# Kernel optimization log

Measured on AMD Instinct MI355X. Metric: run time of the kernel, lower is better.

Reference implementation:

```python
import jax, jax.numpy as jnp
import numpy as np

N_DENSE = 13
N_SPARSE = 26
FIELD_FEAT = 10000
FIELD_NUM = N_DENSE + N_SPARSE  # 39
FEATURE_NUM = N_DENSE + N_SPARSE * FIELD_FEAT  # 260013
K = 16
BATCH = 4096


def setup_inputs() -> dict:
    key = jax.random.key(0)
    k1, k2, k3, k4 = jax.random.split(key, 4)
    dense = jax.random.uniform(k1, (BATCH, N_DENSE), dtype=jnp.float32)
    sparse = jax.random.randint(k2, (BATCH, N_SPARSE), 0, FIELD_FEAT).astype(jnp.float32)
    x = jnp.concatenate([dense, sparse], axis=1)  # [B, field_num]
    # xavier-ish scale for embeddings
    W = jax.random.normal(k3, (FIELD_NUM, FEATURE_NUM, K), dtype=jnp.float32) * 0.01
    fc_w = jax.random.normal(k4, (FEATURE_NUM, 1), dtype=jnp.float32) * 0.01
    bias = jnp.zeros((1,), dtype=jnp.float32)
    field_features = np.array([1] * N_DENSE + [FIELD_FEAT] * N_SPARSE)
    offsets = jnp.asarray(np.concatenate([[0], np.cumsum(field_features)[:-1]]), dtype=jnp.int32)
    return {"x": x, "W": W, "fc_w": fc_w, "bias": bias, "offsets": offsets, "n_dense": N_DENSE}


def reference(x, W, fc_w, bias, offsets, n_dense):
    B, F = x.shape
    # build global feature indices: dense columns -> index 0 (+offset), sparse keep value
    idx = jnp.floor(x).astype(jnp.int32)
    idx = idx.at[:, :n_dense].set(0)
    x_f = idx + offsets[None, :]  # [B, F]
    # field-aware gather: E[i, b, j] = W[i][x_f[b, j]]  -> [F, B, F, K]
    E = jnp.take(W, x_f, axis=1)
    # pairwise dots: dot[b, i, j] = <E[i, b, j], E[j, b, i]>
    dot = jnp.einsum('ibjk,jbik->bij', E, E)  # [B, F, F]
    # multiplier: dense value for dense fields, 1 for sparse fields
    x_m = jnp.concatenate([x[:, :n_dense], jnp.ones((B, F - n_dense), dtype=x.dtype)], axis=1)
    w_pair = x_m[:, :, None] * x_m[:, None, :]  # [B, F, F]
    # original loops: i in [0, F-2], j in [0, F-1] (full j range, faithfully kept)
    row_mask = (jnp.arange(F) < F - 1).astype(x.dtype)[None, :, None]  # [1, F, 1]
    cross = jnp.sum(dot * w_pair * row_mask, axis=(1, 2), keepdims=False)[:, None]  # [B, 1]
    linear = jnp.sum(fc_w[x_f], axis=1) + bias  # [B, 1]
    return jax.nn.sigmoid(linear + cross)
```

## Files before the change

kernel.cpp:

```cpp
#include <hip/hip_runtime.h>
#include <math.h>

#define NF 39
#define ND 13
#define KDIM 16
#define FEAT 260013
#define NPAIRS (NF * (NF + 1) / 2)
#define PASSES ((NPAIRS + 31) / 32)

__global__ __launch_bounds__(256) void ffm_kernel(
    const float* __restrict__ x,
    const float* __restrict__ W,
    const float* __restrict__ fc_w,
    const float* __restrict__ bias,
    const int*   __restrict__ offsets,
    float* __restrict__ out,
    int B)
{
    __shared__ int            sf[NF];
    __shared__ float          sxm[NF];
    __shared__ unsigned short spij[NPAIRS];
    __shared__ float          sred[4];

    const int b   = blockIdx.x;
    const int tid = threadIdx.x;

    if (tid < NF) {
        float xv = x[(size_t)b * NF + tid];
        int idx  = (tid < ND) ? 0 : (int)floorf(xv);
        sf[tid]  = idx + offsets[tid];
        sxm[tid] = (tid < ND) ? xv : 1.0f;
    }
    for (int p = tid; p < NPAIRS; p += 256) {
        int i = 0, base = 0;
        while (p >= base + (NF - i)) { base += NF - i; ++i; }
        int j = i + (p - base);
        spij[p] = (unsigned short)(i | (j << 8));
    }
    __syncthreads();

    const int slot = tid >> 3;
    const int quad = (tid >> 2) & 1;
    const int qi   = tid & 3;

    float acc = 0.0f;
    if (tid < NF) acc += fc_w[sf[tid]];

    #pragma unroll 5
    for (int pass = 0; pass < PASSES; ++pass) {
        int p  = pass * 32 + slot;
        int pc = (p < NPAIRS) ? p : (NPAIRS - 1);
        int ij = spij[pc];
        int i  = ij & 0xff;
        int j  = ij >> 8;

        float w;
        if (i == j)            w = (i < NF - 1) ? sxm[i] * sxm[i] : 0.0f;
        else if (j < NF - 1)   w = 2.0f * sxm[i] * sxm[j];
        else                   w = sxm[i] * sxm[j];
        if (p >= NPAIRS) w = 0.0f;

        int row  = quad ? j : i;
        int feat = quad ? sf[i] : sf[j];
        const float4* vp = (const float4*)(W + ((size_t)row * FEAT + feat) * KDIM);
        float4 v = vp[qi];

        float4 u;
        u.x = __shfl_xor(v.x, 4, 64);
        u.y = __shfl_xor(v.y, 4, 64);
        u.z = __shfl_xor(v.z, 4, 64);
        u.w = __shfl_xor(v.w, 4, 64);

        float d = v.x * u.x + v.y * u.y + v.z * u.z + v.w * u.w;
        acc += 0.5f * w * d;
    }

    #pragma unroll
    for (int off = 32; off > 0; off >>= 1)
        acc += __shfl_down(acc, off, 64);
    if ((tid & 63) == 0) sred[tid >> 6] = acc;
    __syncthreads();

    if (tid == 0) {
        float z = sred[0] + sred[1] + sred[2] + sred[3] + bias[0];
        out[b] = 1.0f / (1.0f + expf(-z));
    }
}

extern "C" void kernel_launch(void* const* d_in, const int* in_sizes, int n_in,
                              void* d_out, int out_size, void* d_ws, size_t ws_size,
                              hipStream_t stream) {
    const float* x       = (const float*)d_in[0];
    const float* W       = (const float*)d_in[1];
    const float* fc_w    = (const float*)d_in[2];
    const float* bias    = (const float*)d_in[3];
    const int*   offsets = (const int*)d_in[4];

    float* out = (float*)d_out;
    const int B = in_sizes[0] / NF;

    ffm_kernel<<<B, 256, 0, stream>>>(x, W, fc_w, bias, offsets, out, B);
}
```

Baseline: 781.3 us.

## Transpose embedding table to feature-major layout before the FFM gather

Adds a kernel that rewrites W from field-major [39][FEAT][16] into feature-major [FEAT][39][16] in the workspace. The main kernel can then load each sparse feature's full 39-field embedding row as one contiguous 2.5KB chunk into shared memory, instead of issuing many scattered 64-byte gathers. Pair weights are precomputed into shared memory and each pair is handled by 4 lanes with float4 loads. The cost is a full read and write of the roughly 650MB table on every call, and the new path only runs when the workspace is large enough. Otherwise it falls back to the old kernel.

```diff
diff --git a/kernel.cpp b/kernel.cpp
--- a/kernel.cpp
+++ b/kernel.cpp
@@ -3,19 +3,140 @@
 
 #define NF 39
 #define ND 13
+#define NS 26
 #define KDIM 16
 #define FEAT 260013
 #define NPAIRS (NF * (NF + 1) / 2)
-#define PASSES ((NPAIRS + 31) / 32)
-
-__global__ __launch_bounds__(256) void ffm_kernel(
+
+#define ROWF4 4
+#define CHUNKF4 (NF * ROWF4)
+#define CHUNKF4_PAD 157
+#define PAIR_SLOTS 832
+#define CPASSES 13
+#define TFEAT 26
+#define TROWF4 (TFEAT * ROWF4)
+#define TROWF4_PAD 105
+
+__global__ __launch_bounds__(256) void ffm_transpose(
+    const float4* __restrict__ W4,
+    float4* __restrict__ WT4)
+{
+    __shared__ float4 sT[NF * TROWF4_PAD];
+    const int fbase = blockIdx.x * TFEAT;
+    const int tid   = threadIdx.x;
+
+    #pragma unroll 8
+    for (int r = tid; r < NF * TROWF4; r += 256) {
+        int row = r / TROWF4;
+        int w   = r - row * TROWF4;
+        if (fbase + (w >> 2) < FEAT)
+            sT[row * TROWF4_PAD + w] = W4[((size_t)row * FEAT + fbase) * 4 + w];
+    }
+    __syncthreads();
+
+    #pragma unroll 8
+    for (int o = tid; o < TFEAT * CHUNKF4; o += 256) {
+        int fl  = o / CHUNKF4;
+        int rem = o - fl * CHUNKF4;
+        int i   = rem >> 2;
+        int k4  = rem & 3;
+        int f   = fbase + fl;
+        if (f < FEAT)
+            WT4[(size_t)f * CHUNKF4 + rem] = sT[i * TROWF4_PAD + (fl << 2) + k4];
+    }
+}
+
+__global__ __launch_bounds__(256) void ffm_main(
     const float* __restrict__ x,
-    const float* __restrict__ W,
+    const float4* __restrict__ WT4,
     const float* __restrict__ fc_w,
     const float* __restrict__ bias,
     const int*   __restrict__ offsets,
     float* __restrict__ out,
     int B)
+{
+    __shared__ float4         sC[NS * CHUNKF4_PAD];
+    __shared__ int            sgb[NF];
+    __shared__ int            sfeat[NF];
+    __shared__ float          sxm[NF];
+    __shared__ unsigned short spij[PAIR_SLOTS];
+    __shared__ float          sw[PAIR_SLOTS];
+    __shared__ float          sred[4];
+
+    const int b   = blockIdx.x;
+    const int tid = threadIdx.x;
+
+    if (tid < NF) {
+        float xv   = x[(size_t)b * NF + tid];
+        int idx    = (tid < ND) ? 0 : (int)floorf(xv);
+        int f      = idx + offsets[tid];
+        sfeat[tid] = f;
+        sgb[tid]   = f * CHUNKF4;
+        sxm[tid]   = (tid < ND) ? xv : 1.0f;
+    }
+    __syncthreads();
+
+    float acc = 0.0f;
+    if (tid < NF) acc += fc_w[sfeat[tid]];
+
+    for (int p = tid; p < PAIR_SLOTS; p += 256) {
+        int i = 0, j = 0; float w = 0.0f;
+        if (p < NPAIRS) {
+            int base = 0, ii = 0;
+            while (p >= base + (NF - ii)) { base += NF - ii; ++ii; }
+            i = ii; j = ii + (p - base);
+            if (i == j)          w = (i < NF - 1) ? sxm[i] * sxm[i] : 0.0f;
+            else if (j < NF - 1) w = 2.0f * sxm[i] * sxm[j];
+            else                 w = sxm[i] * sxm[j];
+        }
+        spij[p] = (unsigned short)(i | (j << 8));
+        sw[p]   = w;
+    }
+
+    #pragma unroll 8
+    for (int t = tid; t < NS * CHUNKF4; t += 256) {
+        int c = t / CHUNKF4;
+        int w = t - c * CHUNKF4;
+        sC[c * CHUNKF4_PAD + w] = WT4[(size_t)sgb[ND + c] + w];
+    }
+    __syncthreads();
+
+    const int slot = tid >> 2;
+    const int q    = tid & 3;
+
+    #pragma unroll 4
+    for (int pass = 0; pass < CPASSES; ++pass) {
+        int   p   = pass * 64 + slot;
+        int   ij  = spij[p];
+        int   i   = ij & 0xff;
+        int   j   = ij >> 8;
+        float wgt = sw[p];
+
+        float4 a = (j >= ND) ? sC[(j - ND) * CHUNKF4_PAD + (i << 2) + q]
+                             : WT4[(size_t)sgb[j] + (i << 2) + q];
+        float4 v = (i >= ND) ? sC[(i - ND) * CHUNKF4_PAD + (j << 2) + q]
+                             : WT4[(size_t)sgb[i] + (j << 2) + q];
+
+        acc += wgt * (a.x * v.x + a.y * v.y + a.z * v.z + a.w * v.w);
+    }
+
+    #pragma unroll
+    for (int off = 32; off > 0; off >>= 1)
+        acc += __shfl_down(acc, off, 64);
+    if ((tid & 63) == 0) sred[tid >> 6] = acc;
+    __syncthreads();
+
+    if (tid == 0) {
+        float z = sred[0] + sred[1] + sred[2] + sred[3] + bias[0];
+        out[b] = 1.0f / (1.0f + expf(-z));
+    }
+}
+
+#define PASSES ((NPAIRS + 31) / 32)
+__global__ __launch_bounds__(256) void ffm_kernel(
+    const float* __restrict__ x, const float* __restrict__ W,
+    const float* __restrict__ fc_w, const float* __restrict__ bias,
+    const int* __restrict__ offsets, float* __restrict__ out, int B)
 {
     __shared__ int            sf[NF];
     __shared__ float          sxm[NF];
@@ -55,9 +176,9 @@
         int j  = ij >> 8;
 
         float w;
-        if (i == j)            w = (i < NF - 1) ? sxm[i] * sxm[i] : 0.0f;
-        else if (j < NF - 1)   w = 2.0f * sxm[i] * sxm[j];
-        else                   w = sxm[i] * sxm[j];
+        if (i == j)          w = (i < NF - 1) ? sxm[i] * sxm[i] : 0.0f;
+        else if (j < NF - 1) w = 2.0f * sxm[i] * sxm[j];
+        else                 w = sxm[i] * sxm[j];
         if (p >= NPAIRS) w = 0.0f;
 
         int row  = quad ? j : i;
@@ -99,5 +220,15 @@
     float* out = (float*)d_out;
     const int B = in_sizes[0] / NF;
 
-    ffm_kernel<<<B, 256, 0, stream>>>(x, W, fc_w, bias, offsets, out, B);
-}
+    const size_t WT_BYTES = (size_t)FEAT * NF * KDIM * sizeof(float);
+
+    if (d_ws != nullptr && ws_size >= WT_BYTES) {
+        float4* WT4 = (float4*)d_ws;
+        const int tgrid = (FEAT + TFEAT - 1) / TFEAT;
+        ffm_transpose<<<tgrid, 256, 0, stream>>>((const float4*)W, WT4);
+        ffm_main<<<B, 256, 0, stream>>>(x, (const float4*)WT4, fc_w, bias,
+                                        offsets, out, B);
+    } else {
+        ffm_kernel<<<B, 256, 0, stream>>>(x, W, fc_w, bias, offsets, out, B);
+    }
+}
```

Result: slower. 1.218 ms (+55.9%).

## Split FFM into prep, pair-major gather kernel with batch tiles, and finalize

Applied to the files above, without the earlier changes.

Replaces the per-sample kernel with three kernels. A prep kernel transposes feature indices. A pair-major kernel processes groups of field pairs over batch tiles, so each block gathers only from two W rows. A final kernel adds the linear term and sigmoid. The intent is better locality in the embedding gathers. In exchange it adds extra launches, shared-memory staging with syncs per pair, and atomic accumulation across batch splits.

```diff
diff --git a/kernel.cpp b/kernel.cpp
--- a/kernel.cpp
+++ b/kernel.cpp
@@ -6,16 +6,130 @@
 #define KDIM 16
 #define FEAT 260013
 #define NPAIRS (NF * (NF + 1) / 2)
+
+#define G_PAIRS 5
+#define PAIR_GROUPS ((NPAIRS + G_PAIRS - 1) / G_PAIRS)
+#define SPLIT 4
+#define SBMAX 1024
+#define PTHREADS 256
+
+__global__ __launch_bounds__(256) void ffm_prep(
+    const float* __restrict__ x, const int* __restrict__ offsets,
+    int* __restrict__ xfeat, float* __restrict__ xd,
+    float* __restrict__ cross, int B)
+{
+    int b = blockIdx.x * 256 + threadIdx.x;
+    if (b >= B) return;
+    #pragma unroll
+    for (int jj = 0; jj < NF; ++jj) {
+        float xv = x[(size_t)b * NF + jj];
+        int idx  = (jj < ND) ? 0 : (int)floorf(xv);
+        xfeat[jj * B + b] = idx + offsets[jj];
+        if (jj < ND) xd[jj * B + b] = xv;
+    }
+    cross[b] = 0.0f;
+}
+
+__global__ __launch_bounds__(PTHREADS) void ffm_pairs(
+    const float4* __restrict__ W4,
+    const int*    __restrict__ xfeat,
+    const float*  __restrict__ xd,
+    float*        __restrict__ cross,
+    int B, int SB)
+{
+    __shared__ float sacc[SBMAX];
+    __shared__ int   sfi[SBMAX];
+    __shared__ int   sfj[SBMAX];
+    __shared__ float smi[SBMAX];
+    __shared__ float smj[SBMAX];
+
+    const int tid   = threadIdx.x;
+    const int pg    = blockIdx.x / SPLIT;
+    const int sp    = blockIdx.x - pg * SPLIT;
+    const int sbase = sp * SB;
+    const int scount = (B - sbase < SB) ? (B - sbase) : SB;
+    if (scount <= 0) return;
+
+    for (int s = tid; s < SBMAX; s += PTHREADS) sacc[s] = 0.0f;
+
+    const int slot = tid >> 3;
+    const int quad = (tid >> 2) & 1;
+
+    for (int g = 0; g < G_PAIRS; ++g) {
+        const int p = pg * G_PAIRS + g;
+        if (p >= NPAIRS) break;
+
+        int i = 0, base = 0;
+        while (p >= base + (NF - i)) { base += NF - i; ++i; }
+        const int j = i + (p - base);
+        float wst;
+        if (i == j)          wst = (i < NF - 1) ? 1.0f : 0.0f;
+        else if (j < NF - 1) wst = 2.0f;
+        else                 wst = 1.0f;
+
+        __syncthreads();
+        for (int s = tid; s < scount; s += PTHREADS) {
+            sfi[s] = xfeat[i * B + sbase + s];
+            sfj[s] = xfeat[j * B + sbase + s];
+            smi[s] = (i < ND) ? xd[i * B + sbase + s] : 1.0f;
+            smj[s] = (j < ND) ? xd[j * B + sbase + s] : 1.0f;
+        }
+        __syncthreads();
+
+        const size_t rowU = (size_t)i * FEAT;
+        const size_t rowV = (size_t)j * FEAT;
+        const int iters = (scount + 31) >> 5;
+
+        #pragma unroll 4
+        for (int it = 0; it < iters; ++it) {
+            int  s     = (it << 5) + slot;
+            bool valid = s < scount;
+            int  sc    = valid ? s : 0;
+
+            int    f    = quad ? sfi[sc] : sfj[sc];
+            size_t base4 = ((quad ? rowV : rowU) + f) * 4 + (tid & 3);
+            float4 v = W4[base4];
+
+            float4 u;
+            u.x = __shfl_xor(v.x, 4, 64);
+            u.y = __shfl_xor(v.y, 4, 64);
+            u.z = __shfl_xor(v.z, 4, 64);
+            u.w = __shfl_xor(v.w, 4, 64);
+
+            float d = v.x * u.x + v.y * u.y + v.z * u.z + v.w * u.w;
+            d += __shfl_xor(d, 1, 64);
+            d += __shfl_xor(d, 2, 64);
+
+            if (valid && (tid & 7) == 0)
+                sacc[sc] += wst * smi[sc] * smj[sc] * d;
+        }
+    }
+
+    __syncthreads();
+    for (int s = tid; s < scount; s += PTHREADS)
+        atomicAdd(&cross[sbase + s], sacc[s]);
+}
+
+__global__ __launch_bounds__(256) void ffm_final(
+    const int*   __restrict__ xfeat, const float* __restrict__ cross,
+    const float* __restrict__ fc_w,  const float* __restrict__ bias,
+    float* __restrict__ out, int B)
+{
+    int b = blockIdx.x * 256 + threadIdx.x;
+    if (b >= B) return;
+    float lin = 0.0f;
+    #pragma unroll
+    for (int jj = 0; jj < NF; ++jj)
+        lin += fc_w[xfeat[jj * B + b]];
+    float z = lin + cross[b] + bias[0];
+    out[b] = 1.0f / (1.0f + expf(-z));
+}
+
 #define PASSES ((NPAIRS + 31) / 32)
-
 __global__ __launch_bounds__(256) void ffm_kernel(
-    const float* __restrict__ x,
-    const float* __restrict__ W,
-    const float* __restrict__ fc_w,
-    const float* __restrict__ bias,
-    const int*   __restrict__ offsets,
-    float* __restrict__ out,
-    int B)
+    const float* __restrict__ x, const float* __restrict__ W,
+    const float* __restrict__ fc_w, const float* __restrict__ bias,
+    const int* __restrict__ offsets, float* __restrict__ out, int B)
 {
     __shared__ int            sf[NF];
     __shared__ float          sxm[NF];
@@ -55,9 +169,9 @@
         int j  = ij >> 8;
 
         float w;
-        if (i == j)            w = (i < NF - 1) ? sxm[i] * sxm[i] : 0.0f;
-        else if (j < NF - 1)   w = 2.0f * sxm[i] * sxm[j];
-        else                   w = sxm[i] * sxm[j];
+        if (i == j)          w = (i < NF - 1) ? sxm[i] * sxm[i] : 0.0f;
+        else if (j < NF - 1) w = 2.0f * sxm[i] * sxm[j];
+        else                 w = sxm[i] * sxm[j];
         if (p >= NPAIRS) w = 0.0f;
 
         int row  = quad ? j : i;
@@ -99,5 +213,24 @@
     float* out = (float*)d_out;
     const int B = in_sizes[0] / NF;
 
-    ffm_kernel<<<B, 256, 0, stream>>>(x, W, fc_w, bias, offsets, out, B);
-}
+    const size_t XF_BYTES = (size_t)NF * B * sizeof(int);
+    const size_t XD_BYTES = (size_t)ND * B * sizeof(float);
+    const size_t CR_BYTES = (size_t)B * sizeof(float);
+    const size_t NEED     = XF_BYTES + XD_BYTES + CR_BYTES + 256;
+
+    if (d_ws != nullptr && ws_size >= NEED && B <= SBMAX * SPLIT) {
+        int*   xfeat = (int*)d_ws;
+        float* xd    = (float*)((char*)d_ws + XF_BYTES);
+        float* cross = (float*)((char*)d_ws + XF_BYTES + XD_BYTES);
+
+        const int SB = (B + SPLIT - 1) / SPLIT;
+        const int pb = (B + 255) / 256;
+
+        ffm_prep<<<pb, 256, 0, stream>>>(x, offsets, xfeat, xd, cross, B);
+        ffm_pairs<<<PAIR_GROUPS * SPLIT, PTHREADS, 0, stream>>>(
+            (const float4*)W, xfeat, xd, cross, B, SB);
+        ffm_final<<<pb, 256, 0, stream>>>(xfeat, cross, fc_w, bias, out, B);
+    } else {
+        ffm_kernel<<<B, 256, 0, stream>>>(x, W, fc_w, bias, offsets, out, B);
+    }
+}
```

Measured after the change: 834.8 us. +6.8%, slower.
